# Optimization experiments

Measured on AMD Instinct MI355X. Metric: run time of the kernel, lower is better.

## Reference

```python
import jax, jax.numpy as jnp
import numpy as np

N_EL = 16
N_NUC = 4
N_FEATS = 32
CUTOFF = 10.0
ION_POT = 0.5
ALPHA = 1.0
BATCH = 32768
HIDDEN = 64
I_IDX, J_IDX = np.triu_indices(N_EL, 1)  # electron pairs i<j
N_PAIRS = N_EL * N_NUC + N_EL * (N_EL - 1) // 2
D_IN = N_PAIRS * N_FEATS


def ssp(x):
    # shifted softplus: softplus(x) - log(2), so ssp(0) = 0
    return jax.nn.softplus(x) - jnp.log(2.0).astype(x.dtype)


def setup_inputs() -> dict:
    key = jax.random.key(0)
    ks = jax.random.split(key, 9)
    rs = jax.random.normal(ks[0], (BATCH, N_EL, 3), jnp.float32) * 2.0
    coords = jax.random.normal(ks[1], (N_NUC, 3), jnp.float32)
    charges = jnp.arange(1, N_NUC + 1, dtype=jnp.float32)
    W1 = jax.random.normal(ks[2], (D_IN, HIDDEN), jnp.float32) / jnp.sqrt(D_IN)
    b1 = jnp.zeros((HIDDEN,), jnp.float32)
    W2 = jax.random.normal(ks[3], (HIDDEN, HIDDEN), jnp.float32) / jnp.sqrt(HIDDEN)
    b2 = jnp.zeros((HIDDEN,), jnp.float32)
    W3 = jax.random.normal(ks[4], (HIDDEN, 1), jnp.float32) / jnp.sqrt(HIDDEN)
    b3 = jnp.zeros((1,), jnp.float32)
    return {"rs": rs, "coords": coords, "charges": charges,
            "W1": W1, "b1": b1, "W2": W2, "b2": b2, "W3": W3, "b3": b3}


def reference(rs, coords, charges, W1, b1, W2, b2, W3, b3):
    B = rs.shape[0]
    # electron-nucleus distances: [B, n_el, n_nuc]
    diff_nuc = rs[:, :, None, :] - coords[None, None, :, :]
    dists_nuc = jnp.sqrt(jnp.sum(diff_nuc * diff_nuc, axis=-1))
    # electron-electron distances for pairs i<j: [B, n_el*(n_el-1)//2]
    diff_el = rs[:, I_IDX, :] - rs[:, J_IDX, :]
    dists_el = jnp.sqrt(jnp.sum(diff_el * diff_el, axis=-1))
    dists = jnp.concatenate([dists_nuc.reshape(B, -1), dists_el], axis=1)  # [B, N_PAIRS]
    # Gaussian distance basis expansion
    qs = jnp.linspace(0.0, 1.0, N_FEATS, dtype=rs.dtype)
    mus = CUTOFF * qs ** 2
    sigmas = (1.0 + CUTOFF * qs) / 7.0
    xs = jnp.exp(-((dists[..., None] - mus) ** 2) / sigmas ** 2)  # [B, N_PAIRS, N_FEATS]
    xs = xs.reshape(B, -1)
    # small MLP with shifted-softplus activations
    h = ssp(xs @ W1 + b1)
    h = ssp(h @ W2 + b2)
    ys = (h @ W3 + b3)[:, 0]
    # nuclear asymptotic factor
    decay = jnp.sqrt(2.0 * ION_POT)
    terms = (charges[None, None, :] * dists_nuc + decay * ALPHA * dists_nuc ** 2) / (1.0 + ALPHA * dists_nuc)
    asymp = jnp.exp(-jnp.sum(terms, axis=(1, 2)))
    return jnp.exp(ys) * asymp
```

## Files before the change

kernel.cpp:

```cpp
#include <hip/hip_runtime.h>
#include <math.h>

#define N_EL    16
#define N_NUC   4
#define N_FEATS 32
#define N_PAIRS 184
#define HIDDEN  64
#define TB      32
#define BLOCK   256
#define DLD     185
#define H1LD    68
#define TPW     23

typedef int   intx8    __attribute__((ext_vector_type(8)));
typedef float floatx16 __attribute__((ext_vector_type(16)));

__device__ __forceinline__ float exp2_raw(float x) {
    float r;
    asm("v_exp_f32 %0, %1" : "=v"(r) : "v"(x));
    return r;
}

__constant__ unsigned char c_I[120] = {
    0,0,0,0,0,0,0,0,0,0,0,0,0,0,0,
    1,1,1,1,1,1,1,1,1,1,1,1,1,1,
    2,2,2,2,2,2,2,2,2,2,2,2,2,
    3,3,3,3,3,3,3,3,3,3,3,3,
    4,4,4,4,4,4,4,4,4,4,4,
    5,5,5,5,5,5,5,5,5,5,
    6,6,6,6,6,6,6,6,6,
    7,7,7,7,7,7,7,7,
    8,8,8,8,8,8,8,
    9,9,9,9,9,9,
    10,10,10,10,10,
    11,11,11,11,
    12,12,12,
    13,13,
    14
};
__constant__ unsigned char c_J[120] = {
    1,2,3,4,5,6,7,8,9,10,11,12,13,14,15,
    2,3,4,5,6,7,8,9,10,11,12,13,14,15,
    3,4,5,6,7,8,9,10,11,12,13,14,15,
    4,5,6,7,8,9,10,11,12,13,14,15,
    5,6,7,8,9,10,11,12,13,14,15,
    6,7,8,9,10,11,12,13,14,15,
    7,8,9,10,11,12,13,14,15,
    8,9,10,11,12,13,14,15,
    9,10,11,12,13,14,15,
    10,11,12,13,14,15,
    11,12,13,14,15,
    12,13,14,15,
    13,14,15,
    14,15,
    15
};

__device__ __forceinline__ float ssp(float x) {
    float a = fabsf(x);
    return fmaxf(x, 0.0f) + log1pf(__expf(-a)) - 0.69314718056f;
}
__device__ __forceinline__ float redg(float v) {
    v += __shfl_xor(v, 1);
    v += __shfl_xor(v, 2);
    v += __shfl_xor(v, 4);
    return v;
}

__global__ __launch_bounds__(256)
void prep_w1_kernel(const float* __restrict__ W1, intx8* __restrict__ ws)
{
    __shared__ float w[2 * N_FEATS * HIDDEN];
    const int t = blockIdx.x;
    const float* src = W1 + (size_t)(2 * t) * (N_FEATS * HIDDEN);
    for (int k = threadIdx.x; k < 2 * N_FEATS * HIDDEN; k += 256) w[k] = src[k];
    __syncthreads();

    const int tid = threadIdx.x;
    if (tid >= 128) return;
    const int lane = tid & 63;
    const int nh   = tid >> 6;
    const int lh   = lane >> 5;
    const int col  = nh * 32 + (lane & 31);
    const int fb   = lh * 16;
    intx8 frag;
#pragma unroll
    for (int r = 0; r < 8; ++r) {
        const int pair = r >> 2;
        const int fo   = fb + ((r & 3) << 2);
        const float v0 = 64.0f * w[(pair * N_FEATS + fo + 0) * 64 + col];
        const float v1 = 64.0f * w[(pair * N_FEATS + fo + 1) * 64 + col];
        const float v2 = 64.0f * w[(pair * N_FEATS + fo + 2) * 64 + col];
        const float v3 = 64.0f * w[(pair * N_FEATS + fo + 3) * 64 + col];
        int d = __builtin_amdgcn_cvt_pk_fp8_f32(v0, v1, 0, false);
        d     = __builtin_amdgcn_cvt_pk_fp8_f32(v2, v3, d, true);
        frag[r] = d;
    }
    ws[(size_t)(t * 2 + nh) * 64 + lane] = frag;
}

__global__ __launch_bounds__(BLOCK)
void wfnet_kernel(const float* __restrict__ rs,
                  const float* __restrict__ coords,
                  const float* __restrict__ charges,
                  const intx8* __restrict__ ws,
                  const float* __restrict__ b1,
                  const float* __restrict__ W2,
                  const float* __restrict__ b2,
                  const float* __restrict__ W3,
                  const float* __restrict__ b3,
                  float* __restrict__ out)
{
    __shared__ float lds_rs[TB * N_EL * 3];
    __shared__ float lds_dist[TB * DLD];

    const int tid  = threadIdx.x;
    const int wave = tid >> 6;
    const int lane = tid & 63;
    const int m    = lane & 31;
    const int lh   = lane >> 5;

    {
        const float* rs_blk = rs + (size_t)blockIdx.x * (TB * N_EL * 3);
        for (int k = tid; k < TB * N_EL * 3; k += BLOCK) lds_rs[k] = rs_blk[k];
    }
    __syncthreads();

    float asy = 0.0f;
    {
        const int bl = tid >> 3, g = tid & 7;
        const float* myrs = lds_rs + bl * (N_EL * 3);
        float* dst = lds_dist + bl * DLD;
        const float4 ch = *(const float4*)charges;
        for (int i = 0; i < 8; ++i) {
            const int p = g + 8 * i;
            const int e = p >> 2, n = p & 3;
            const float dx = myrs[e * 3 + 0] - coords[n * 3 + 0];
            const float dy = myrs[e * 3 + 1] - coords[n * 3 + 1];
            const float dz = myrs[e * 3 + 2] - coords[n * 3 + 2];
            const float d = sqrtf(dx * dx + dy * dy + dz * dz);
            dst[p] = d;
            const float Z = (n < 2) ? ((n == 0) ? ch.x : ch.y)
                                    : ((n == 2) ? ch.z : ch.w);
            asy += (Z * d + d * d) / (1.0f + d);
        }
        for (int i = 0; i < 15; ++i) {
            const int q  = g + 8 * i;
            const int ei = 3 * (int)c_I[q], ej = 3 * (int)c_J[q];
            const float dx = myrs[ei + 0] - myrs[ej + 0];
            const float dy = myrs[ei + 1] - myrs[ej + 1];
            const float dz = myrs[ei + 2] - myrs[ej + 2];
            dst[64 + q] = sqrtf(dx * dx + dy * dy + dz * dz);
        }
    }
    __syncthreads();

    const int f0 = lh * 16;
#define MKC(P, FF) float P##1, P##0; { \
    const float fq = (float)(FF) * (1.0f / 31.0f); \
    const float mu = 10.0f * fq * fq; \
    const float is = 7.0f / (1.0f + 10.0f * fq); \
    P##1 = is * 1.2011224087864498f; \
    P##0 = -mu * P##1; }
    MKC(F0_,  f0 + 0)  MKC(F1_,  f0 + 1)  MKC(F2_,  f0 + 2)  MKC(F3_,  f0 + 3)
    MKC(F4_,  f0 + 4)  MKC(F5_,  f0 + 5)  MKC(F6_,  f0 + 6)  MKC(F7_,  f0 + 7)
    MKC(F8_,  f0 + 8)  MKC(F9_,  f0 + 9)  MKC(F10_, f0 + 10) MKC(F11_, f0 + 11)
    MKC(F12_, f0 + 12) MKC(F13_, f0 + 13) MKC(F14_, f0 + 14) MKC(F15_, f0 + 15)
#undef MKC

    floatx16 accA = {};
    floatx16 accB = {};
    const intx8* wq = ws + ((size_t)(wave * TPW) * 128 + lane);
    const float* drow = lds_dist + m * DLD + wave * (2 * TPW);

#define XO(dd, P) ({ const float t_ = fmaf(dd, P##1, P##0); exp2_raw(t_ * -t_); })
#define MKA8(AV, dx0, dx1) \
    intx8 AV; { int dw_; \
    dw_   = __builtin_amdgcn_cvt_pk_fp8_f32(XO(dx0,F0_),  XO(dx0,F1_),  0,  false); \
    AV[0] = __builtin_amdgcn_cvt_pk_fp8_f32(XO(dx0,F2_),  XO(dx0,F3_),  dw_, true); \
    dw_   = __builtin_amdgcn_cvt_pk_fp8_f32(XO(dx0,F4_),  XO(dx0,F5_),  0,  false); \
    AV[1] = __builtin_amdgcn_cvt_pk_fp8_f32(XO(dx0,F6_),  XO(dx0,F7_),  dw_, true); \
    dw_   = __builtin_amdgcn_cvt_pk_fp8_f32(XO(dx0,F8_),  XO(dx0,F9_),  0,  false); \
    AV[2] = __builtin_amdgcn_cvt_pk_fp8_f32(XO(dx0,F10_), XO(dx0,F11_), dw_, true); \
    dw_   = __builtin_amdgcn_cvt_pk_fp8_f32(XO(dx0,F12_), XO(dx0,F13_), 0,  false); \
    AV[3] = __builtin_amdgcn_cvt_pk_fp8_f32(XO(dx0,F14_), XO(dx0,F15_), dw_, true); \
    dw_   = __builtin_amdgcn_cvt_pk_fp8_f32(XO(dx1,F0_),  XO(dx1,F1_),  0,  false); \
    AV[4] = __builtin_amdgcn_cvt_pk_fp8_f32(XO(dx1,F2_),  XO(dx1,F3_),  dw_, true); \
    dw_   = __builtin_amdgcn_cvt_pk_fp8_f32(XO(dx1,F4_),  XO(dx1,F5_),  0,  false); \
    AV[5] = __builtin_amdgcn_cvt_pk_fp8_f32(XO(dx1,F6_),  XO(dx1,F7_),  dw_, true); \
    dw_   = __builtin_amdgcn_cvt_pk_fp8_f32(XO(dx1,F8_),  XO(dx1,F9_),  0,  false); \
    AV[6] = __builtin_amdgcn_cvt_pk_fp8_f32(XO(dx1,F10_), XO(dx1,F11_), dw_, true); \
    dw_   = __builtin_amdgcn_cvt_pk_fp8_f32(XO(dx1,F12_), XO(dx1,F13_), 0,  false); \
    AV[7] = __builtin_amdgcn_cvt_pk_fp8_f32(XO(dx1,F14_), XO(dx1,F15_), dw_, true); }
#define KROUND(AV, Q0, Q1) { \
    accA = __builtin_amdgcn_mfma_scale_f32_32x32x64_f8f6f4( \
               AV, Q0, accA, 0, 0, 0, 0x7F7F7F7F, 0, 0x79797979); \
    accB = __builtin_amdgcn_mfma_scale_f32_32x32x64_f8f6f4( \
               AV, Q1, accB, 0, 0, 0, 0x7F7F7F7F, 0, 0x79797979); }

    intx8 pA0 = wq[0],   pA1 = wq[64];
    intx8 pB0 = wq[128], pB1 = wq[192];
    float dA0 = drow[0], dA1 = drow[1];
    float dB0 = drow[2], dB1 = drow[3];

    for (int it = 0; it < 10; ++it) {
        const intx8* wn = wq + 256;
        const float eA0 = drow[4 * it + 4], eA1 = drow[4 * it + 5];
        const float eB0 = drow[4 * it + 6], eB1 = drow[4 * it + 7];

        { MKA8(av, dA0, dA1) KROUND(av, pA0, pA1) }
        pA0 = wn[0]; pA1 = wn[64];

        { MKA8(bv, dB0, dB1) KROUND(bv, pB0, pB1) }
        pB0 = wn[128]; pB1 = wn[192];

        wq = wn;
        dA0 = eA0; dA1 = eA1; dB0 = eB0; dB1 = eB1;
    }
    {
        const intx8* wn = wq + 256;
        const float eA0 = drow[44], eA1 = drow[45];
        { MKA8(av, dA0, dA1) KROUND(av, pA0, pA1) }
        pA0 = wn[0]; pA1 = wn[64];
        { MKA8(bv, dB0, dB1) KROUND(bv, pB0, pB1) }
        { MKA8(cv, eA0, eA1) KROUND(cv, pA0, pA1) }
    }
#undef KROUND
#undef MKA8
#undef XO

    __syncthreads();
    float* lds_red = lds_dist;

    if (wave >= 2) {
        float* dst = lds_red + (wave - 2) * 2048;
#pragma unroll
        for (int rg = 0; rg < 16; ++rg) {
            const int el = (rg & 3) + 8 * (rg >> 2) + 4 * lh;
            dst[el * 64 + m]      = accA[rg];
            dst[el * 64 + 32 + m] = accB[rg];
        }
    }
    __syncthreads();
    if (wave < 2) {
        const float* srcr = lds_red + wave * 2048;
#pragma unroll
        for (int rg = 0; rg < 16; ++rg) {
            const int el = (rg & 3) + 8 * (rg >> 2) + 4 * lh;
            accA[rg] += srcr[el * 64 + m];
            accB[rg] += srcr[el * 64 + 32 + m];
        }
    }
    __syncthreads();
    if (wave == 1) {
#pragma unroll
        for (int rg = 0; rg < 16; ++rg) {
            const int el = (rg & 3) + 8 * (rg >> 2) + 4 * lh;
            lds_red[el * 64 + m]      = accA[rg];
            lds_red[el * 64 + 32 + m] = accB[rg];
        }
    }
    __syncthreads();
    if (wave == 0) {
        const float bA = b1[m], bB = b1[32 + m];
#pragma unroll
        for (int rg = 0; rg < 16; ++rg) {
            const int el = (rg & 3) + 8 * (rg >> 2) + 4 * lh;
            accA[rg] += lds_red[el * 64 + m];
            accB[rg] += lds_red[el * 64 + 32 + m];
        }
#pragma unroll
        for (int rg = 0; rg < 16; ++rg) {
            const int el = (rg & 3) + 8 * (rg >> 2) + 4 * lh;
            lds_red[el * H1LD + m]      = ssp(accA[rg] + bA);
            lds_red[el * H1LD + 32 + m] = ssp(accB[rg] + bB);
        }
    }
    __syncthreads();

    const int b_local = tid >> 3;
    const int g       = tid & 7;
    const int b       = blockIdx.x * TB + b_local;
    asy = redg(asy);

    const float4* __restrict__ W2v = (const float4*)W2;
    const float4* __restrict__ b2v = (const float4*)b2;
    const int wbi = g * 2;
    const float4 b2a = b2v[wbi], b2b = b2v[wbi + 1];
    float s0 = b2a.x, s1 = b2a.y, s2 = b2a.z, s3 = b2a.w;
    float s4 = b2b.x, s5 = b2b.y, s6 = b2b.z, s7 = b2b.w;

    const float* __restrict__ h1row = lds_red + b_local * H1LD;
    for (int k = 0; k < HIDDEN; ++k) {
        const float hk  = h1row[k];
        const float4 wa = W2v[k * 16 + wbi];
        const float4 wb = W2v[k * 16 + wbi + 1];
        s0 = fmaf(hk, wa.x, s0); s1 = fmaf(hk, wa.y, s1);
        s2 = fmaf(hk, wa.z, s2); s3 = fmaf(hk, wa.w, s3);
        s4 = fmaf(hk, wb.x, s4); s5 = fmaf(hk, wb.y, s5);
        s6 = fmaf(hk, wb.z, s6); s7 = fmaf(hk, wb.w, s7);
    }

    const float4* __restrict__ W3v = (const float4*)W3;
    const float4 w3a = W3v[wbi], w3b = W3v[wbi + 1];
    float part = ssp(s0) * w3a.x + ssp(s1) * w3a.y
               + ssp(s2) * w3a.z + ssp(s3) * w3a.w
               + ssp(s4) * w3b.x + ssp(s5) * w3b.y
               + ssp(s6) * w3b.z + ssp(s7) * w3b.w;
    part = redg(part);

    if (g == 0) {
        const float ys = part + b3[0];
        out[b] = __expf(ys) * __expf(-asy);
    }
}

extern "C" void kernel_launch(void* const* d_in, const int* in_sizes, int n_in,
                              void* d_out, int out_size, void* d_ws, size_t ws_size,
                              hipStream_t stream) {
    const float* rs      = (const float*)d_in[0];
    const float* coords  = (const float*)d_in[1];
    const float* charges = (const float*)d_in[2];
    const float* W1      = (const float*)d_in[3];
    const float* b1      = (const float*)d_in[4];
    const float* W2      = (const float*)d_in[5];
    const float* b2      = (const float*)d_in[6];
    const float* W3      = (const float*)d_in[7];
    const float* b3      = (const float*)d_in[8];
    float* out = (float*)d_out;

    const int batch = in_sizes[0] / (N_EL * 3);
    intx8* ws = (intx8*)d_ws;

    prep_w1_kernel<<<N_PAIRS / 2, 256, 0, stream>>>(W1, ws);
    wfnet_kernel<<<batch / TB, BLOCK, 0, stream>>>(rs, coords, charges, ws,
                                                   b1, W2, b2, W3, b3, out);
}
```

Before: 158.1 us.

## Split fused kernel into GEMM and tail kernels via global partial sums

Splits the monolithic kernel into two: a GEMM kernel that writes each wave's layer-1 partial accumulators to global workspace, and a tail kernel that sums the four partials, applies bias and softplus, recomputes the nuclear asymptotic term and runs layers 2 and 3. This removes the multi-stage LDS cross-wave reduction and its barriers from the GEMM kernel, which may shrink its register and LDS footprint and raise occupancy. In exchange it adds a 32 KB-per-block round trip through global memory (about 128 MB of writes and reads in total), an extra kernel launch, and recomputation of the electron-nucleus distances.

```diff
diff --git a/kernel.cpp b/kernel.cpp
--- a/kernel.cpp
+++ b/kernel.cpp
@@ -11,6 +11,7 @@
 #define DLD     185
 #define H1LD    68
 #define TPW     23
+#define WS_PART_OFF (1 << 19)
 
 typedef int   intx8    __attribute__((ext_vector_type(8)));
 typedef float floatx16 __attribute__((ext_vector_type(16)));
@@ -100,16 +101,10 @@
 }
 
 __global__ __launch_bounds__(BLOCK)
-void wfnet_kernel(const float* __restrict__ rs,
-                  const float* __restrict__ coords,
-                  const float* __restrict__ charges,
-                  const intx8* __restrict__ ws,
-                  const float* __restrict__ b1,
-                  const float* __restrict__ W2,
-                  const float* __restrict__ b2,
-                  const float* __restrict__ W3,
-                  const float* __restrict__ b3,
-                  float* __restrict__ out)
+void wfnet_gemm(const float* __restrict__ rs,
+                const float* __restrict__ coords,
+                const intx8* __restrict__ ws,
+                float* __restrict__ partials)
 {
     __shared__ float lds_rs[TB * N_EL * 3];
     __shared__ float lds_dist[TB * DLD];
@@ -126,23 +121,17 @@
     }
     __syncthreads();
 
-    float asy = 0.0f;
     {
         const int bl = tid >> 3, g = tid & 7;
         const float* myrs = lds_rs + bl * (N_EL * 3);
         float* dst = lds_dist + bl * DLD;
-        const float4 ch = *(const float4*)charges;
         for (int i = 0; i < 8; ++i) {
             const int p = g + 8 * i;
             const int e = p >> 2, n = p & 3;
             const float dx = myrs[e * 3 + 0] - coords[n * 3 + 0];
             const float dy = myrs[e * 3 + 1] - coords[n * 3 + 1];
             const float dz = myrs[e * 3 + 2] - coords[n * 3 + 2];
-            const float d = sqrtf(dx * dx + dy * dy + dz * dz);
-            dst[p] = d;
-            const float Z = (n < 2) ? ((n == 0) ? ch.x : ch.y)
-                                    : ((n == 2) ? ch.z : ch.w);
-            asy += (Z * d + d * d) / (1.0f + d);
+            dst[p] = sqrtf(dx * dx + dy * dy + dz * dz);
         }
         for (int i = 0; i < 15; ++i) {
             const int q  = g + 8 * i;
@@ -229,58 +218,81 @@
 #undef MKA8
 #undef XO
 
+    float* pdst = partials + ((size_t)blockIdx.x * 4 + wave) * 2048;
+#pragma unroll
+    for (int rg = 0; rg < 16; ++rg) {
+        const int el = (rg & 3) + 8 * (rg >> 2) + 4 * lh;
+        pdst[el * 64 + m]      = accA[rg];
+        pdst[el * 64 + 32 + m] = accB[rg];
+    }
+}
+
+__global__ __launch_bounds__(BLOCK)
+void wfnet_tail(const float* __restrict__ rs,
+                const float* __restrict__ coords,
+                const float* __restrict__ charges,
+                const float* __restrict__ partials,
+                const float* __restrict__ b1,
+                const float* __restrict__ W2,
+                const float* __restrict__ b2,
+                const float* __restrict__ W3,
+                const float* __restrict__ b3,
+                float* __restrict__ out)
+{
+    __shared__ float lds_rs[TB * N_EL * 3];
+    __shared__ float lds_h1[TB * H1LD];
+
+    const int tid = threadIdx.x;
+    const int el  = tid >> 3;
+    const int g   = tid & 7;
+    const int b   = blockIdx.x * TB + el;
+
+    {
+        const float* rs_blk = rs + (size_t)blockIdx.x * (TB * N_EL * 3);
+        for (int k = tid; k < TB * N_EL * 3; k += BLOCK) lds_rs[k] = rs_blk[k];
+    }
+
+    {
+        const float* pb = partials + (size_t)blockIdx.x * 8192 + el * 64 + g * 8;
+        const float4 p00 = ((const float4*)(pb + 0 * 2048))[0];
+        const float4 p01 = ((const float4*)(pb + 0 * 2048))[1];
+        const float4 p10 = ((const float4*)(pb + 1 * 2048))[0];
+        const float4 p11 = ((const float4*)(pb + 1 * 2048))[1];
+        const float4 p20 = ((const float4*)(pb + 2 * 2048))[0];
+        const float4 p21 = ((const float4*)(pb + 2 * 2048))[1];
+        const float4 p30 = ((const float4*)(pb + 3 * 2048))[0];
+        const float4 p31 = ((const float4*)(pb + 3 * 2048))[1];
+        const float4 ba = ((const float4*)(b1 + g * 8))[0];
+        const float4 bb = ((const float4*)(b1 + g * 8))[1];
+        float* h1w = lds_h1 + el * H1LD + g * 8;
+        h1w[0] = ssp(p00.x + p10.x + p20.x + p30.x + ba.x);
+        h1w[1] = ssp(p00.y + p10.y + p20.y + p30.y + ba.y);
+        h1w[2] = ssp(p00.z + p10.z + p20.z + p30.z + ba.z);
+        h1w[3] = ssp(p00.w + p10.w + p20.w + p30.w + ba.w);
+        h1w[4] = ssp(p01.x + p11.x + p21.x + p31.x + bb.x);
+        h1w[5] = ssp(p01.y + p11.y + p21.y + p31.y + bb.y);
+        h1w[6] = ssp(p01.z + p11.z + p21.z + p31.z + bb.z);
+        h1w[7] = ssp(p01.w + p11.w + p21.w + p31.w + bb.w);
+    }
+
+    float asy = 0.0f;
     __syncthreads();
-    float* lds_red = lds_dist;
-
-    if (wave >= 2) {
-        float* dst = lds_red + (wave - 2) * 2048;
+    {
+        const float* myrs = lds_rs + el * (N_EL * 3);
+        const float4 ch = *(const float4*)charges;
 #pragma unroll
-        for (int rg = 0; rg < 16; ++rg) {
-            const int el = (rg & 3) + 8 * (rg >> 2) + 4 * lh;
-            dst[el * 64 + m]      = accA[rg];
-            dst[el * 64 + 32 + m] = accB[rg];
+        for (int i = 0; i < 8; ++i) {
+            const int p = g + 8 * i;
+            const int e = p >> 2, n = p & 3;
+            const float dx = myrs[e * 3 + 0] - coords[n * 3 + 0];
+            const float dy = myrs[e * 3 + 1] - coords[n * 3 + 1];
+            const float dz = myrs[e * 3 + 2] - coords[n * 3 + 2];
+            const float d = sqrtf(dx * dx + dy * dy + dz * dz);
+            const float Z = (n < 2) ? ((n == 0) ? ch.x : ch.y)
+                                    : ((n == 2) ? ch.z : ch.w);
+            asy += (Z * d + d * d) / (1.0f + d);
         }
     }
-    __syncthreads();
-    if (wave < 2) {
-        const float* srcr = lds_red + wave * 2048;
-#pragma unroll
-        for (int rg = 0; rg < 16; ++rg) {
-            const int el = (rg & 3) + 8 * (rg >> 2) + 4 * lh;
-            accA[rg] += srcr[el * 64 + m];
-            accB[rg] += srcr[el * 64 + 32 + m];
-        }
-    }
-    __syncthreads();
-    if (wave == 1) {
-#pragma unroll
-        for (int rg = 0; rg < 16; ++rg) {
-            const int el = (rg & 3) + 8 * (rg >> 2) + 4 * lh;
-            lds_red[el * 64 + m]      = accA[rg];
-            lds_red[el * 64 + 32 + m] = accB[rg];
-        }
-    }
-    __syncthreads();
-    if (wave == 0) {
-        const float bA = b1[m], bB = b1[32 + m];
-#pragma unroll
-        for (int rg = 0; rg < 16; ++rg) {
-            const int el = (rg & 3) + 8 * (rg >> 2) + 4 * lh;
-            accA[rg] += lds_red[el * 64 + m];
-            accB[rg] += lds_red[el * 64 + 32 + m];
-        }
-#pragma unroll
-        for (int rg = 0; rg < 16; ++rg) {
-            const int el = (rg & 3) + 8 * (rg >> 2) + 4 * lh;
-            lds_red[el * H1LD + m]      = ssp(accA[rg] + bA);
-            lds_red[el * H1LD + 32 + m] = ssp(accB[rg] + bB);
-        }
-    }
-    __syncthreads();
-
-    const int b_local = tid >> 3;
-    const int g       = tid & 7;
-    const int b       = blockIdx.x * TB + b_local;
     asy = redg(asy);
 
     const float4* __restrict__ W2v = (const float4*)W2;
@@ -290,7 +302,7 @@
     float s0 = b2a.x, s1 = b2a.y, s2 = b2a.z, s3 = b2a.w;
     float s4 = b2b.x, s5 = b2b.y, s6 = b2b.z, s7 = b2b.w;
 
-    const float* __restrict__ h1row = lds_red + b_local * H1LD;
+    const float* __restrict__ h1row = lds_h1 + el * H1LD;
     for (int k = 0; k < HIDDEN; ++k) {
         const float hk  = h1row[k];
         const float4 wa = W2v[k * 16 + wbi];
@@ -330,9 +342,11 @@
     float* out = (float*)d_out;
 
     const int batch = in_sizes[0] / (N_EL * 3);
-    intx8* ws = (intx8*)d_ws;
-
-    prep_w1_kernel<<<N_PAIRS / 2, 256, 0, stream>>>(W1, ws);
-    wfnet_kernel<<<batch / TB, BLOCK, 0, stream>>>(rs, coords, charges, ws,
-                                                   b1, W2, b2, W3, b3, out);
-}
+    intx8* w1f8     = (intx8*)d_ws;
+    float* partials = (float*)((char*)d_ws + WS_PART_OFF);
+
+    prep_w1_kernel<<<N_PAIRS / 2, 256, 0, stream>>>(W1, w1f8);
+    wfnet_gemm<<<batch / TB, BLOCK, 0, stream>>>(rs, coords, w1f8, partials);
+    wfnet_tail<<<batch / TB, BLOCK, 0, stream>>>(rs, coords, charges, partials,
+                                                 b1, W2, b2, W3, b3, out);
+}
```

Measured after the change: 147.0 us. 1.08x faster.
